# Optimization experiments

Measured on AMD Instinct MI355X. Metric: run time of the kernel, lower is better.

The kernel has to match this reference:

```python
import jax, jax.numpy as jnp
import numpy as np

B, S, OUT = 128, 3000, 84
CODE_SEQ = 30
LAT = 1024
C, D = 128, 16
CB = C * D  # 2048
IN = CODE_SEQ * OUT  # 2520


def setup_inputs() -> dict:
    key = jax.random.key(0)
    ks = jax.random.split(key, 16)
    def w(k, shape):
        fan_in = shape[0]
        return (jax.random.normal(k, shape, dtype=jnp.float32) / np.sqrt(fan_in)).astype(jnp.float32)
    return {
        "y": jax.random.normal(ks[0], (B, S, OUT), dtype=jnp.float32),
        "emb": jax.random.uniform(ks[1], (C, D), minval=-1.0 / C, maxval=1.0 / C, dtype=jnp.float32),
        "eW1": w(ks[2], (IN, LAT)), "eb1": jnp.zeros((LAT,), jnp.float32),
        "eW2": w(ks[3], (LAT, LAT)), "eb2": jnp.zeros((LAT,), jnp.float32),
        "eW3": w(ks[4], (LAT, CB)), "eb3": jnp.zeros((CB,), jnp.float32),
        "dW1": w(ks[5], (CB, LAT)), "db1": jnp.zeros((LAT,), jnp.float32),
        "dW2": w(ks[6], (LAT, LAT)), "db2": jnp.zeros((LAT,), jnp.float32),
        "dW3": w(ks[7], (LAT, IN)), "db3": jnp.zeros((IN,), jnp.float32),
    }


def _mlp(z, W1, b1, W2, b2, W3, b3):
    # LinearEncoder in eval mode (dropout = identity): Linear->ELU->Linear->ELU->Linear
    z = jax.nn.elu(z @ W1 + b1)
    z = jax.nn.elu(z @ W2 + b2)
    return z @ W3 + b3


def reference(y, emb, eW1, eb1, eW2, eb2, eW3, eb3, dW1, db1, dW2, db2, dW3, db3):
    batch, seq_len = y.shape[0], y.shape[1]
    # seq_len % code_seq == 0 -> padding branch is a no-op
    y2 = y.reshape(batch, -1, IN)                 # (B, n_m, 2520)
    n_m = y2.shape[1]
    ze = _mlp(y2, eW1, eb1, eW2, eb2, eW3, eb3)   # (B, n_m, 2048)
    zef = ze.reshape(batch, n_m, -1, D)           # (B, n_m, G=128, 16)
    # squared L2 distance to each of C codes, without materializing (B,n_m,G,C,D)
    dist = (
        jnp.sum(zef ** 2, -1, keepdims=True)
        - 2.0 * jnp.einsum("bngd,cd->bngc", zef, emb)
        + jnp.sum(emb ** 2, -1)
    )                                             # (B, n_m, G, C)
    nn_idx = jnp.argmin(dist, -1)                 # (B, n_m, G)
    zq = emb[nn_idx].reshape(batch, n_m, -1)      # (B, n_m, 2048)
    dec_in = ze + jax.lax.stop_gradient(zq - ze)  # straight-through
    out = _mlp(dec_in, dW1, db1, dW2, db2, dW3, db3)
    out = out.reshape(batch, -1, OUT)[:, :seq_len, :]
    return (out, ze, zq)
```

## Files before the change

kernel.cpp:

```cpp
#include <hip/hip_runtime.h>
#include <hip/hip_bf16.h>
#include <cstdint>
#include <cstddef>

typedef __bf16 bf16_t;
typedef bf16_t bf16x8 __attribute__((ext_vector_type(8)));
typedef float  f32x4  __attribute__((ext_vector_type(4)));

__device__ __forceinline__ void gl_lds16(const void* g, void* l) {
  __builtin_amdgcn_global_load_lds(
      (const __attribute__((address_space(1))) void*)g,
      (__attribute__((address_space(3))) void*)l, 16, 0, 0);
}

#define BAR()  __builtin_amdgcn_s_barrier()
#define LGK0() asm volatile("s_waitcnt lgkmcnt(0)" ::: "memory")

__device__ __forceinline__ void transpose_tile(
    const float* __restrict__ W, bf16_t* __restrict__ Wt,
    int K, int N, int Kpad, int Npad, int bx, int by, int t)
{
  __shared__ float tile[32][33];
  const int tx = t & 31, ty = t >> 5;
  const int k0 = bx * 32, n0 = by * 32;
#pragma unroll
  for (int i = 0; i < 4; ++i) {
    int k = k0 + ty + i * 8, n = n0 + tx;
    tile[ty + i * 8][tx] = (k < K && n < N) ? W[(size_t)k * N + n] : 0.f;
  }
  __syncthreads();
#pragma unroll
  for (int i = 0; i < 4; ++i) {
    int n = n0 + ty + i * 8, k = k0 + tx;
    if (n < Npad && k < Kpad)
      Wt[(size_t)n * Kpad + k] = (bf16_t)tile[tx][ty + i * 8];
  }
}

__global__ __launch_bounds__(256) void prep_kernel(
    const float* __restrict__ y, bf16_t* __restrict__ X0,
    const float* __restrict__ eW1, bf16_t* __restrict__ W1t,
    const float* __restrict__ eW2, bf16_t* __restrict__ W2t,
    const float* __restrict__ eW3, bf16_t* __restrict__ W3t,
    const float* __restrict__ dW1, bf16_t* __restrict__ V1t,
    const float* __restrict__ dW2, bf16_t* __restrict__ V2t,
    const float* __restrict__ dW3, bf16_t* __restrict__ V3t)
{
  const int b = blockIdx.x;
  const int t = threadIdx.x;
  if (b < 16000) {
    const int idx = b * 256 + t;
    const int r = idx / 320, c = (idx % 320) * 8;
    bf16x8 v;
    if (c < 2520) {
      const float4 f0 = *(const float4*)(y + (size_t)r * 2520 + c);
      const float4 f1 = *(const float4*)(y + (size_t)r * 2520 + c + 4);
      v[0] = (bf16_t)f0.x; v[1] = (bf16_t)f0.y; v[2] = (bf16_t)f0.z; v[3] = (bf16_t)f0.w;
      v[4] = (bf16_t)f1.x; v[5] = (bf16_t)f1.y; v[6] = (bf16_t)f1.z; v[7] = (bf16_t)f1.w;
    } else {
#pragma unroll
      for (int j = 0; j < 8; ++j) v[j] = (bf16_t)0.f;
    }
    *(bf16x8*)(X0 + (size_t)r * 2560 + c) = v;
    return;
  }
  int lb = b - 16000;
  if (lb < 2560)      { transpose_tile(eW1, W1t, 2520, 1024, 2560, 1024, lb % 80, lb / 80, t); return; }
  lb -= 2560;
  if (lb < 1024)      { transpose_tile(eW2, W2t, 1024, 1024, 1024, 1024, lb % 32, lb / 32, t); return; }
  lb -= 1024;
  if (lb < 2048)      { transpose_tile(eW3, W3t, 1024, 2048, 1024, 2048, lb % 32, lb / 32, t); return; }
  lb -= 2048;
  if (lb < 2048)      { transpose_tile(dW1, V1t, 2048, 1024, 2048, 1024, lb % 64, lb / 64, t); return; }
  lb -= 2048;
  if (lb < 1024)      { transpose_tile(dW2, V2t, 1024, 1024, 1024, 1024, lb % 32, lb / 32, t); return; }
  lb -= 1024;
  transpose_tile(dW3, V3t, 1024, 2520, 1024, 2560, lb % 32, lb / 32, t);
}

__device__ __forceinline__ bf16x8 ldsfrag(const bf16_t* half_, int r, int kc, int kg) {
  int lin = (r << 7) + (kc << 6) + (kg << 4);
  lin ^= ((lin >> 9) & 1) << 5;
  return *(const bf16x8*)((const char*)half_ + lin);
}

template<int ELU>
__global__ __launch_bounds__(512, 2) void gemm256(
    const bf16_t* __restrict__ A, const bf16_t* __restrict__ Bt,
    const float* __restrict__ bias,
    bf16_t* __restrict__ Cb, float* __restrict__ Cf,
    int M, int N, int K, int Nlog)
{
  __shared__ __align__(16) bf16_t lds[65536];

  const int t  = threadIdx.x;
  const int w  = t >> 6, l = t & 63;
  const int fr = l & 15, kg = l >> 4;
  const int wm = (w >> 2) * 128, wn = (w & 3) * 64;
  const int bro = (wn & 64);

  const int gx = gridDim.x;
  const int nwg = gx * (int)gridDim.y;
  int lin = blockIdx.y * gx + blockIdx.x;
  int q8 = nwg >> 3, r8 = nwg & 7, xcd = lin & 7, idx = lin >> 3;
  int swz = (xcd < r8 ? xcd * (q8 + 1) : r8 * (q8 + 1) + (xcd - r8) * q8) + idx;
  const int tn = (swz % gx) * 256;
  const int tm = (swz / gx) * 256;

  const int srow = w * 8 + (l >> 3);
  const int sce  = ((l & 7) * 8) ^ (((l >> 5) & 1) << 4);
  const int sdst = w * 512 + l * 8;

  const int NT = K >> 6;

  f32x4 acc[8][4];
#pragma unroll
  for (int i = 0; i < 8; ++i)
#pragma unroll
    for (int j = 0; j < 4; ++j) acc[i][j] = (f32x4){0.f, 0.f, 0.f, 0.f};

  auto stage = [&](const bf16_t* gbase, bf16_t* lhalf) {
    gl_lds16(gbase + (size_t)srow * K + sce,        lhalf + sdst);
    gl_lds16(gbase + (size_t)(srow + 64) * K + sce, lhalf + 4096 + sdst);
  };

  stage(A  + (size_t)tm * K,          lds);
  stage(A  + (size_t)(tm + 128) * K,  lds + 8192);
  stage(Bt + (size_t)tn * K,          lds + 16384);
  stage(Bt + (size_t)(tn + 128) * K,  lds + 16384 + 8192);
  asm volatile("s_waitcnt vmcnt(0)" ::: "memory");
  BAR();

  for (int kt = 0; kt < NT; ++kt) {
    const int s = kt & 1;
    const bf16_t* aH = lds + s * 32768 + (wm >> 7) * 8192;
    const bf16_t* bH = lds + s * 32768 + 16384 + (wn >> 7) * 8192;
    bf16_t* aNx = lds + (s ^ 1) * 32768;
    bf16_t* bNx = aNx + 16384;
    const bool pf = (kt + 1 < NT);
    const size_t kn = (size_t)(kt + 1) << 6;

    bf16x8 af[4][2], bf_[2][2];

#pragma unroll
    for (int mi = 0; mi < 4; ++mi)
#pragma unroll
      for (int kc = 0; kc < 2; ++kc)
        af[mi][kc] = ldsfrag(aH, mi * 16 + fr, kc, kg);
    asm volatile("s_waitcnt vmcnt(0)" ::: "memory");
    BAR();
#pragma unroll
    for (int nj = 0; nj < 2; ++nj)
#pragma unroll
      for (int kc = 0; kc < 2; ++kc)
        bf_[nj][kc] = ldsfrag(bH, bro + nj * 16 + fr, kc, kg);
    if (pf) stage(A + (size_t)tm * K + kn, aNx);
    BAR(); LGK0();
    __builtin_amdgcn_s_setprio(1);
#pragma unroll
    for (int mi = 0; mi < 4; ++mi)
#pragma unroll
      for (int nj = 0; nj < 2; ++nj)
#pragma unroll
        for (int kc = 0; kc < 2; ++kc)
          acc[mi][nj] = __builtin_amdgcn_mfma_f32_16x16x32_bf16(af[mi][kc], bf_[nj][kc], acc[mi][nj], 0, 0, 0);
    __builtin_amdgcn_s_setprio(0);
    BAR();

#pragma unroll
    for (int nj = 0; nj < 2; ++nj)
#pragma unroll
      for (int kc = 0; kc < 2; ++kc)
        bf_[nj][kc] = ldsfrag(bH, bro + (nj + 2) * 16 + fr, kc, kg);
    if (pf) stage(A + (size_t)(tm + 128) * K + kn, aNx + 8192);
    BAR(); LGK0();
    __builtin_amdgcn_s_setprio(1);
#pragma unroll
    for (int mi = 0; mi < 4; ++mi)
#pragma unroll
      for (int nj = 0; nj < 2; ++nj)
#pragma unroll
        for (int kc = 0; kc < 2; ++kc)
          acc[mi][nj + 2] = __builtin_amdgcn_mfma_f32_16x16x32_bf16(af[mi][kc], bf_[nj][kc], acc[mi][nj + 2], 0, 0, 0);
    __builtin_amdgcn_s_setprio(0);
    BAR();

#pragma unroll
    for (int mi = 0; mi < 4; ++mi)
#pragma unroll
      for (int kc = 0; kc < 2; ++kc)
        af[mi][kc] = ldsfrag(aH, (mi + 4) * 16 + fr, kc, kg);
    if (pf) stage(Bt + (size_t)tn * K + kn, bNx);
    BAR(); LGK0();
    __builtin_amdgcn_s_setprio(1);
#pragma unroll
    for (int mi = 0; mi < 4; ++mi)
#pragma unroll
      for (int nj = 0; nj < 2; ++nj)
#pragma unroll
        for (int kc = 0; kc < 2; ++kc)
          acc[mi + 4][nj + 2] = __builtin_amdgcn_mfma_f32_16x16x32_bf16(af[mi][kc], bf_[nj][kc], acc[mi + 4][nj + 2], 0, 0, 0);
    __builtin_amdgcn_s_setprio(0);
    BAR();

#pragma unroll
    for (int nj = 0; nj < 2; ++nj)
#pragma unroll
      for (int kc = 0; kc < 2; ++kc)
        bf_[nj][kc] = ldsfrag(bH, bro + nj * 16 + fr, kc, kg);
    if (pf) stage(Bt + (size_t)(tn + 128) * K + kn, bNx + 8192);
    asm volatile("s_waitcnt vmcnt(4)" ::: "memory");
    BAR(); LGK0();
    __builtin_amdgcn_s_setprio(1);
#pragma unroll
    for (int mi = 0; mi < 4; ++mi)
#pragma unroll
      for (int nj = 0; nj < 2; ++nj)
#pragma unroll
        for (int kc = 0; kc < 2; ++kc)
          acc[mi + 4][nj] = __builtin_amdgcn_mfma_f32_16x16x32_bf16(af[mi][kc], bf_[nj][kc], acc[mi + 4][nj], 0, 0, 0);
    __builtin_amdgcn_s_setprio(0);
    BAR();
  }

#pragma unroll
  for (int mi = 0; mi < 8; ++mi) {
    const int row0 = tm + wm + mi * 16 + kg * 4;
#pragma unroll
    for (int nj = 0; nj < 4; ++nj) {
      const int col = tn + wn + nj * 16 + fr;
      const float bv = (col < Nlog) ? bias[col] : 0.f;
#pragma unroll
      for (int r = 0; r < 4; ++r) {
        float v = acc[mi][nj][r] + bv;
        if (ELU) v = (v > 0.f) ? v : expm1f(v);
        const int row = row0 + r;
        if (Cb) Cb[(size_t)row * N + col] = (bf16_t)v;
        if (Cf && col < Nlog) Cf[(size_t)row * Nlog + col] = v;
      }
    }
  }
}

__global__ __launch_bounds__(256) void vq_mfma(
    const float* __restrict__ ze, const float* __restrict__ emb,
    float* __restrict__ zq, bf16_t* __restrict__ zqb)
{
  __shared__ float  se[2048];
  __shared__ bf16_t seb[2048];
  const int t = threadIdx.x;
  for (int i = t; i < 2048; i += 256) { float v = emb[i]; se[i] = v; seb[i] = (bf16_t)v; }
  __syncthreads();

  const int l = t & 63, w = t >> 6;
  const int col = l & 15;
  const int ks8 = (l >> 4) * 8;
  const bool kact = (ks8 < 16);

  bf16x8 bfrag[8];
  float  hv[8];
#pragma unroll
  for (int cb = 0; cb < 8; ++cb) {
    float s = 0.f;
    bf16x8 bf;
#pragma unroll
    for (int j = 0; j < 8; ++j) bf[j] = (bf16_t)0.f;
    if (kact) {
      const float* ep = se + (cb * 16 + col) * 16 + ks8;
      float4 e0 = *(const float4*)ep;
      float4 e1 = *(const float4*)(ep + 4);
      bf[0] = (bf16_t)e0.x; bf[1] = (bf16_t)e0.y; bf[2] = (bf16_t)e0.z; bf[3] = (bf16_t)e0.w;
      bf[4] = (bf16_t)e1.x; bf[5] = (bf16_t)e1.y; bf[6] = (bf16_t)e1.z; bf[7] = (bf16_t)e1.w;
      s = e0.x*e0.x + e0.y*e0.y + e0.z*e0.z + e0.w*e0.w
        + e1.x*e1.x + e1.y*e1.y + e1.z*e1.z + e1.w*e1.w;
    }
    s += __shfl_xor(s, 16);
    s += __shfl_xor(s, 32);
    bfrag[cb] = bf;
    hv[cb] = 0.5f * s;
  }

  const int base_tile = blockIdx.x * 64 + w * 16;
  for (int it = 0; it < 16; ++it) {
    const int tile = base_tile + it;
    const int row = tile >> 3, g0 = (tile & 7) * 16;

    bf16x8 afrag;
#pragma unroll
    for (int j = 0; j < 8; ++j) afrag[j] = (bf16_t)0.f;
    if (kact) {
      const float* ap = ze + (size_t)row * 2048 + (g0 + col) * 16 + ks8;
      float4 a0 = *(const float4*)ap;
      float4 a1 = *(const float4*)(ap + 4);
      afrag[0] = (bf16_t)(-a0.x); afrag[1] = (bf16_t)(-a0.y);
      afrag[2] = (bf16_t)(-a0.z); afrag[3] = (bf16_t)(-a0.w);
      afrag[4] = (bf16_t)(-a1.x); afrag[5] = (bf16_t)(-a1.y);
      afrag[6] = (bf16_t)(-a1.z); afrag[7] = (bf16_t)(-a1.w);
    }

    f32x4 dd[8];
#pragma unroll
    for (int cb = 0; cb < 8; ++cb) {
      f32x4 c = (f32x4){hv[cb], hv[cb], hv[cb], hv[cb]};
      dd[cb] = __builtin_amdgcn_mfma_f32_16x16x32_bf16(afrag, bfrag[cb], c, 0, 0, 0);
    }

#pragma unroll
    for (int r = 0; r < 4; ++r) {
      float bd = dd[0][r]; int bi = col;
#pragma unroll
      for (int cb = 1; cb < 8; ++cb) {
        float v = dd[cb][r];
        int   ci = cb * 16 + col;
        if (v < bd) { bd = v; bi = ci; }
      }
#pragma unroll
      for (int m = 1; m < 16; m <<= 1) {
        float od = __shfl_xor(bd, m);
        int   oi = __shfl_xor(bi, m);
        if (od < bd || (od == bd && oi < bi)) { bd = od; bi = oi; }
      }
      if (col == r) {
        const int tok = (l >> 4) * 4 + r;
        const size_t go = ((size_t)row * 128 + g0 + tok) * 16;
        const float*  e  = se  + bi * 16;
        const bf16_t* eb = seb + bi * 16;
#pragma unroll
        for (int v = 0; v < 4; ++v)
          *(float4*)(zq + go + v * 4) = ((const float4*)e)[v];
        *(bf16x8*)(zqb + go)     = ((const bf16x8*)eb)[0];
        *(bf16x8*)(zqb + go + 8) = ((const bf16x8*)eb)[1];
      }
    }
  }
}

extern "C" void kernel_launch(void* const* d_in, const int* in_sizes, int n_in,
                              void* d_out, int out_size, void* d_ws, size_t ws_size,
                              hipStream_t stream)
{
  const float* y   = (const float*)d_in[0];
  const float* emb = (const float*)d_in[1];
  const float* eW1 = (const float*)d_in[2];
  const float* eb1 = (const float*)d_in[3];
  const float* eW2 = (const float*)d_in[4];
  const float* eb2 = (const float*)d_in[5];
  const float* eW3 = (const float*)d_in[6];
  const float* eb3 = (const float*)d_in[7];
  const float* dW1 = (const float*)d_in[8];
  const float* db1 = (const float*)d_in[9];
  const float* dW2 = (const float*)d_in[10];
  const float* db2 = (const float*)d_in[11];
  const float* dW3 = (const float*)d_in[12];
  const float* db3 = (const float*)d_in[13];

  float* out = (float*)d_out;
  float* ze  = out + 32256000;
  float* zq  = ze + 26214400;

  uint8_t* ws = (uint8_t*)d_ws;
  size_t off = 0;
  auto alloc = [&](size_t bytes) -> void* {
    void* p = ws + off; off += (bytes + 255) & ~(size_t)255; return p;
  };
  bf16_t* X0  = (bf16_t*)alloc(12800ULL * 2560 * 2);
  bf16_t* W1t = (bf16_t*)alloc(1024ULL * 2560 * 2);
  bf16_t* W2t = (bf16_t*)alloc(1024ULL * 1024 * 2);
  bf16_t* W3t = (bf16_t*)alloc(2048ULL * 1024 * 2);
  bf16_t* V1t = (bf16_t*)alloc(1024ULL * 2048 * 2);
  bf16_t* V2t = (bf16_t*)alloc(1024ULL * 1024 * 2);
  bf16_t* V3t = (bf16_t*)alloc(2560ULL * 1024 * 2);
  bf16_t* H1  = (bf16_t*)alloc(12800ULL * 1024 * 2);
  bf16_t* H2  = (bf16_t*)alloc(12800ULL * 1024 * 2);
  bf16_t* ZQb = (bf16_t*)alloc(12800ULL * 2048 * 2);

  prep_kernel<<<27264, 256, 0, stream>>>(y, X0, eW1, W1t, eW2, W2t, eW3, W3t,
                                         dW1, V1t, dW2, V2t, dW3, V3t);

  gemm256<1><<<dim3(4, 50), 512, 0, stream>>>(X0, W1t, eb1, H1, nullptr, 12800, 1024, 2560, 1024);
  gemm256<1><<<dim3(4, 50), 512, 0, stream>>>(H1, W2t, eb2, H2, nullptr, 12800, 1024, 1024, 1024);
  gemm256<0><<<dim3(8, 50), 512, 0, stream>>>(H2, W3t, eb3, nullptr, ze, 12800, 2048, 1024, 2048);
  vq_mfma<<<1600, 256, 0, stream>>>(ze, emb, zq, ZQb);
  gemm256<1><<<dim3(4, 50), 512, 0, stream>>>(ZQb, V1t, db1, H1, nullptr, 12800, 1024, 2048, 1024);
  gemm256<1><<<dim3(4, 50), 512, 0, stream>>>(H1, V2t, db2, H2, nullptr, 12800, 1024, 1024, 1024);
  gemm256<0><<<dim3(10, 50), 512, 0, stream>>>(H2, V3t, db3, nullptr, out, 12800, 2560, 1024, 2520);
}
```

Baseline: 679.6 us.

## Switch GEMM mainloop to 4-slot K=32 pipeline with three tiles in flight

Rewrites the gemm256 main loop to use K-steps of 32 instead of 64, with a 4-slot LDS ring buffer and three stages prefetched ahead in place of double buffering. The LDS layout becomes plain unswizzled 64-byte rows, and each iteration now has two compute phases instead of four. The aim is deeper latency hiding for global-to-LDS loads and fewer barriers per MFMA. In exchange it drops the XOR swizzle, which may bring LDS bank conflicts, and it doubles the iteration count with less MFMA work between barriers.

```diff
diff --git a/kernel.cpp b/kernel.cpp
--- a/kernel.cpp
+++ b/kernel.cpp
@@ -78,12 +78,6 @@
   transpose_tile(dW3, V3t, 1024, 2520, 1024, 2560, lb % 32, lb / 32, t);
 }
 
-__device__ __forceinline__ bf16x8 ldsfrag(const bf16_t* half_, int r, int kc, int kg) {
-  int lin = (r << 7) + (kc << 6) + (kg << 4);
-  lin ^= ((lin >> 9) & 1) << 5;
-  return *(const bf16x8*)((const char*)half_ + lin);
-}
-
 template<int ELU>
 __global__ __launch_bounds__(512, 2) void gemm256(
     const bf16_t* __restrict__ A, const bf16_t* __restrict__ Bt,
@@ -97,7 +91,6 @@
   const int w  = t >> 6, l = t & 63;
   const int fr = l & 15, kg = l >> 4;
   const int wm = (w >> 2) * 128, wn = (w & 3) * 64;
-  const int bro = (wn & 64);
 
   const int gx = gridDim.x;
   const int nwg = gx * (int)gridDim.y;
@@ -107,11 +100,11 @@
   const int tn = (swz % gx) * 256;
   const int tm = (swz / gx) * 256;
 
-  const int srow = w * 8 + (l >> 3);
-  const int sce  = ((l & 7) * 8) ^ (((l >> 5) & 1) << 4);
-  const int sdst = w * 512 + l * 8;
-
-  const int NT = K >> 6;
+  const int srow = t >> 2;
+  const int scol = (t & 3) * 8;
+  const int sdst = t * 8;
+
+  const int NT = K >> 5;
 
   f32x4 acc[8][4];
 #pragma unroll
@@ -119,107 +112,63 @@
 #pragma unroll
     for (int j = 0; j < 4; ++j) acc[i][j] = (f32x4){0.f, 0.f, 0.f, 0.f};
 
-  auto stage = [&](const bf16_t* gbase, bf16_t* lhalf) {
-    gl_lds16(gbase + (size_t)srow * K + sce,        lhalf + sdst);
-    gl_lds16(gbase + (size_t)(srow + 64) * K + sce, lhalf + 4096 + sdst);
+  auto stageA = [&](int slot, int kn) {
+    bf16_t* d = lds + slot * 16384;
+    gl_lds16(A + (size_t)(tm + srow) * K + kn + scol,       d + sdst);
+    gl_lds16(A + (size_t)(tm + 128 + srow) * K + kn + scol, d + 4096 + sdst);
   };
-
-  stage(A  + (size_t)tm * K,          lds);
-  stage(A  + (size_t)(tm + 128) * K,  lds + 8192);
-  stage(Bt + (size_t)tn * K,          lds + 16384);
-  stage(Bt + (size_t)(tn + 128) * K,  lds + 16384 + 8192);
-  asm volatile("s_waitcnt vmcnt(0)" ::: "memory");
+  auto stageB = [&](int slot, int kn) {
+    bf16_t* d = lds + slot * 16384 + 8192;
+    gl_lds16(Bt + (size_t)(tn + srow) * K + kn + scol,       d + sdst);
+    gl_lds16(Bt + (size_t)(tn + 128 + srow) * K + kn + scol, d + 4096 + sdst);
+  };
+
+  stageA(0, 0);  stageB(0, 0);
+  stageA(1, 32); stageB(1, 32);
+  stageA(2, 64); stageB(2, 64);
+  asm volatile("s_waitcnt vmcnt(8)" ::: "memory");
   BAR();
 
   for (int kt = 0; kt < NT; ++kt) {
-    const int s = kt & 1;
-    const bf16_t* aH = lds + s * 32768 + (wm >> 7) * 8192;
-    const bf16_t* bH = lds + s * 32768 + 16384 + (wn >> 7) * 8192;
-    bf16_t* aNx = lds + (s ^ 1) * 32768;
-    bf16_t* bNx = aNx + 16384;
-    const bool pf = (kt + 1 < NT);
-    const size_t kn = (size_t)(kt + 1) << 6;
-
-    bf16x8 af[4][2], bf_[2][2];
-
-#pragma unroll
-    for (int mi = 0; mi < 4; ++mi)
-#pragma unroll
-      for (int kc = 0; kc < 2; ++kc)
-        af[mi][kc] = ldsfrag(aH, mi * 16 + fr, kc, kg);
-    asm volatile("s_waitcnt vmcnt(0)" ::: "memory");
-    BAR();
+    const int slot = kt & 3;
+    const bf16_t* aH = lds + slot * 16384 + wm * 32;
+    const bf16_t* bH = lds + slot * 16384 + 8192 + wn * 32;
+    const bool pf = (kt + 3 < NT);
+    const int ps = (kt + 3) & 3;
+    const int kn = (kt + 3) << 5;
+
+    bf16x8 af[8], bf_[2];
+
+#pragma unroll
+    for (int mi = 0; mi < 8; ++mi)
+      af[mi] = *(const bf16x8*)(aH + (mi * 16 + fr) * 32 + kg * 8);
 #pragma unroll
     for (int nj = 0; nj < 2; ++nj)
-#pragma unroll
-      for (int kc = 0; kc < 2; ++kc)
-        bf_[nj][kc] = ldsfrag(bH, bro + nj * 16 + fr, kc, kg);
-    if (pf) stage(A + (size_t)tm * K + kn, aNx);
+      bf_[nj] = *(const bf16x8*)(bH + (nj * 16 + fr) * 32 + kg * 8);
+    if (pf) stageA(ps, kn);
     BAR(); LGK0();
     __builtin_amdgcn_s_setprio(1);
 #pragma unroll
-    for (int mi = 0; mi < 4; ++mi)
+    for (int mi = 0; mi < 8; ++mi)
 #pragma unroll
       for (int nj = 0; nj < 2; ++nj)
-#pragma unroll
-        for (int kc = 0; kc < 2; ++kc)
-          acc[mi][nj] = __builtin_amdgcn_mfma_f32_16x16x32_bf16(af[mi][kc], bf_[nj][kc], acc[mi][nj], 0, 0, 0);
+        acc[mi][nj] = __builtin_amdgcn_mfma_f32_16x16x32_bf16(af[mi], bf_[nj], acc[mi][nj], 0, 0, 0);
     __builtin_amdgcn_s_setprio(0);
     BAR();
 
 #pragma unroll
     for (int nj = 0; nj < 2; ++nj)
-#pragma unroll
-      for (int kc = 0; kc < 2; ++kc)
-        bf_[nj][kc] = ldsfrag(bH, bro + (nj + 2) * 16 + fr, kc, kg);
-    if (pf) stage(A + (size_t)(tm + 128) * K + kn, aNx + 8192);
+      bf_[nj] = *(const bf16x8*)(bH + ((nj + 2) * 16 + fr) * 32 + kg * 8);
+    if (pf) stageB(ps, kn);
     BAR(); LGK0();
     __builtin_amdgcn_s_setprio(1);
 #pragma unroll
-    for (int mi = 0; mi < 4; ++mi)
+    for (int mi = 0; mi < 8; ++mi)
 #pragma unroll
       for (int nj = 0; nj < 2; ++nj)
-#pragma unroll
-        for (int kc = 0; kc < 2; ++kc)
-          acc[mi][nj + 2] = __builtin_amdgcn_mfma_f32_16x16x32_bf16(af[mi][kc], bf_[nj][kc], acc[mi][nj + 2], 0, 0, 0);
+        acc[mi][nj + 2] = __builtin_amdgcn_mfma_f32_16x16x32_bf16(af[mi], bf_[nj], acc[mi][nj + 2], 0, 0, 0);
     __builtin_amdgcn_s_setprio(0);
-    BAR();
-
-#pragma unroll
-    for (int mi = 0; mi < 4; ++mi)
-#pragma unroll
-      for (int kc = 0; kc < 2; ++kc)
-        af[mi][kc] = ldsfrag(aH, (mi + 4) * 16 + fr, kc, kg);
-    if (pf) stage(Bt + (size_t)tn * K + kn, bNx);
-    BAR(); LGK0();
-    __builtin_amdgcn_s_setprio(1);
-#pragma unroll
-    for (int mi = 0; mi < 4; ++mi)
-#pragma unroll
-      for (int nj = 0; nj < 2; ++nj)
-#pragma unroll
-        for (int kc = 0; kc < 2; ++kc)
-          acc[mi + 4][nj + 2] = __builtin_amdgcn_mfma_f32_16x16x32_bf16(af[mi][kc], bf_[nj][kc], acc[mi + 4][nj + 2], 0, 0, 0);
-    __builtin_amdgcn_s_setprio(0);
-    BAR();
-
-#pragma unroll
-    for (int nj = 0; nj < 2; ++nj)
-#pragma unroll
-      for (int kc = 0; kc < 2; ++kc)
-        bf_[nj][kc] = ldsfrag(bH, bro + nj * 16 + fr, kc, kg);
-    if (pf) stage(Bt + (size_t)(tn + 128) * K + kn, bNx + 8192);
-    asm volatile("s_waitcnt vmcnt(4)" ::: "memory");
-    BAR(); LGK0();
-    __builtin_amdgcn_s_setprio(1);
-#pragma unroll
-    for (int mi = 0; mi < 4; ++mi)
-#pragma unroll
-      for (int nj = 0; nj < 2; ++nj)
-#pragma unroll
-        for (int kc = 0; kc < 2; ++kc)
-          acc[mi + 4][nj] = __builtin_amdgcn_mfma_f32_16x16x32_bf16(af[mi][kc], bf_[nj][kc], acc[mi + 4][nj], 0, 0, 0);
-    __builtin_amdgcn_s_setprio(0);
+    asm volatile("s_waitcnt vmcnt(8)" ::: "memory");
     BAR();
   }
 
```

Result: faster. 662.5 us (-2.5%).
